# Optimization experiments

Hardware: AMD Instinct MI355X
Metric: run time of the kernel (lower is better)

Reference implementation:

```python
import jax, jax.numpy as jnp
import numpy as np

T, C, NH, NL, NP = 5, 192, 4, 5, 4
DH = C // NH

def leaky(x):
    return jnp.where(x >= 0, x, 0.1 * x)

def conv2d(x, w, b, padding=1, dilation=1):
    out = jax.lax.conv_general_dilated(
        x, w, window_strides=(1, 1),
        padding=[(padding, padding), (padding, padding)],
        rhs_dilation=(dilation, dilation),
        dimension_numbers=('NCHW', 'OIHW', 'NCHW'))
    return out + b[None, :, None, None]

def grid_sample_border(img, gx, gy):
    # align_corners=True, padding_mode='border'; gx/gy normalized [-1,1], shape (B,H,W)
    B, Cc, H, W = img.shape
    x = jnp.clip((gx + 1.0) * 0.5 * (W - 1), 0.0, W - 1)
    y = jnp.clip((gy + 1.0) * 0.5 * (H - 1), 0.0, H - 1)
    x0 = jnp.floor(x); y0 = jnp.floor(y)
    wx = (x - x0).reshape(B, 1, -1); wy = (y - y0).reshape(B, 1, -1)
    flat = img.reshape(B, Cc, H * W)
    def g(yi, xi):
        xi = jnp.clip(xi, 0, W - 1).astype(jnp.int32)
        yi = jnp.clip(yi, 0, H - 1).astype(jnp.int32)
        return jnp.take_along_axis(flat, (yi * W + xi).reshape(B, 1, -1), axis=2)
    out = (g(y0, x0) * (1 - wx) * (1 - wy) + g(y0, x0 + 1) * wx * (1 - wy)
         + g(y0 + 1, x0) * (1 - wx) * wy + g(y0 + 1, x0 + 1) * wx * wy)
    return out.reshape(B, Cc, H, W)

def warp(x, flo):
    B, _, H, W = x.shape
    xx = jnp.arange(W, dtype=jnp.float32)[None, :] * jnp.ones((H, 1), jnp.float32)
    yy = jnp.arange(H, dtype=jnp.float32)[:, None] * jnp.ones((1, W), jnp.float32)
    gx = 2.0 * (xx[None] + flo[:, 0]) / max(W - 1, 1) - 1.0
    gy = 2.0 * (yy[None] + flo[:, 1]) / max(H - 1, 1) - 1.0
    return grid_sample_border(x, gx, gy)

def deform_sample(v_img, loc):
    # v_img (N,D,H,W); loc (N,Q,P,2) in [0,1]; bilinear, zeros padding, align_corners=False
    N, D, H, W = v_img.shape
    Q, P = loc.shape[1], loc.shape[2]
    x = loc[..., 0] * W - 0.5
    y = loc[..., 1] * H - 0.5
    x0 = jnp.floor(x); y0 = jnp.floor(y)
    wx = (x - x0).reshape(N, 1, -1); wy = (y - y0).reshape(N, 1, -1)
    flat = v_img.reshape(N, D, H * W)
    def g(yi, xi):
        valid = ((xi >= 0) & (xi <= W - 1) & (yi >= 0) & (yi <= H - 1)).astype(v_img.dtype)
        xi_c = jnp.clip(xi, 0, W - 1).astype(jnp.int32)
        yi_c = jnp.clip(yi, 0, H - 1).astype(jnp.int32)
        return jnp.take_along_axis(flat, (yi_c * W + xi_c).reshape(N, 1, -1), axis=2) * valid.reshape(N, 1, -1)
    out = (g(y0, x0) * (1 - wx) * (1 - wy) + g(y0, x0 + 1) * wx * (1 - wy)
         + g(y0 + 1, x0) * (1 - wx) * wy + g(y0 + 1, x0 + 1) * wx * wy)
    return out.reshape(N, D, Q, P)

def _forward(frame, srcframe, flow_forward, flow_backward,
             w_qk, b_qk, w_v, b_v, w_vproj, b_vproj, w_off, b_off,
             w_attn, b_attn, w_out, b_out, w_ff, b_ff,
             w_ffn1, b_ffn1, w_ffn2, b_ffn2):
    b, t, c, h, w = frame.shape
    ff01, ff12 = flow_forward[:, 0], flow_forward[:, 1]
    fb32, fb43 = flow_backward[:, 2], flow_backward[:, 3]
    ff02 = ff01 + warp(ff12, ff01)
    fb42 = fb43 + warp(fb32, fb43)
    warp02 = warp(frame[:, 0], ff02)
    warp12 = warp(frame[:, 1], ff12)
    warp32 = warp(frame[:, 3], fb32)
    warp42 = warp(frame[:, 4], fb42)
    qk_in = jnp.concatenate([warp02, warp12, frame[:, 2], warp32, warp42,
                             flow_forward.reshape(b, -1, h, w),
                             flow_backward.reshape(b, -1, h, w)], axis=1)
    queries = leaky(conv2d(qk_in, w_qk, b_qk)).reshape(b, t, c, h, w)
    value = leaky(conv2d(frame.reshape(b, t * c, h, w), w_v, b_v)).reshape(b, t, c, h, w)

    Lq = t * h * w
    q_tok = queries.transpose(0, 1, 3, 4, 2).reshape(b, Lq, c)
    v_tok = value.transpose(0, 1, 3, 4, 2).reshape(b, Lq, c)
    v_proj = (v_tok @ w_vproj.T + b_vproj).reshape(b, t, h * w, NH, DH)

    offs = (q_tok @ w_off.T + b_off).reshape(b, Lq, NH, NL, NP, 2)
    aw = (q_tok @ w_attn.T + b_attn).reshape(b, Lq, NH, NL * NP)
    aw = jax.nn.softmax(aw, axis=-1).reshape(b, Lq, NH, NL, NP)

    # reference points (all valid ratios are ones): ((x+0.5)/W, (y+0.5)/H)
    rx = (jnp.arange(w, dtype=frame.dtype) + 0.5) / w
    ry = (jnp.arange(h, dtype=frame.dtype) + 0.5) / h
    ref = jnp.stack(jnp.meshgrid(rx, ry, indexing='xy'), axis=-1).reshape(h * w, 2)
    ref = jnp.tile(ref, (t, 1))  # (Lq, 2)

    norm = jnp.array([w, h], dtype=frame.dtype)
    # flow-guided per-level displacement toward the center frame (level 2)
    zero = jnp.zeros_like(ff12)
    flows = jnp.stack([ff02, ff12, zero, fb32, fb42], axis=1)  # (b,NL,2,h,w)
    flow_norm = (flows / norm[None, None, :, None, None]).transpose(0, 1, 3, 4, 2).reshape(b, NL, h * w, 2)
    flow_norm = jnp.tile(flow_norm.transpose(0, 2, 1, 3), (1, t, 1, 1))  # (b,Lq,NL,2)

    loc = (ref[None, :, None, None, None, :]
           + offs / norm[None, None, None, None, None, :]
           + flow_norm[:, :, None, :, None, :])  # (b,Lq,NH,NL,NP,2)

    acc = jnp.zeros((b * NH, DH, Lq), dtype=frame.dtype)
    for l in range(NL):
        v_l = v_proj[:, l].transpose(0, 2, 3, 1).reshape(b * NH, DH, h, w)
        loc_l = loc[:, :, :, l].transpose(0, 2, 1, 3, 4).reshape(b * NH, Lq, NP, 2)
        samp = deform_sample(v_l, loc_l)  # (b*NH, DH, Lq, NP)
        w_l = aw[:, :, :, l].transpose(0, 2, 1, 3).reshape(b * NH, 1, Lq, NP)
        acc = acc + (samp * w_l).sum(-1)
    attn = acc.reshape(b, NH, DH, Lq).transpose(0, 3, 1, 2).reshape(b, Lq, c)
    attn = attn @ w_out.T + b_out

    out = attn.reshape(b, t, h, w, c).transpose(0, 1, 4, 2, 3).reshape(b * t, c, h, w)
    out = conv2d(out, w_ff, b_ff)
    out = out.reshape(b, t, c, h, w) + frame
    seq_in = jnp.concatenate([out.reshape(b * t, c, h, w), srcframe.reshape(b * t, c, h, w)], axis=1)
    ffn = conv2d(seq_in, w_ffn1, b_ffn1, padding=2, dilation=2)
    ffn = conv2d(leaky(ffn), w_ffn2, b_ffn2)
    out = out.reshape(b * t, c, h, w) + ffn
    return out.reshape(b, t, c, h, w)

def setup_inputs():
    key = jax.random.key(0)
    ks = jax.random.split(key, 16)
    B, H, W = 2, 64, 64
    s = 0.02
    d = {}
    d['frame'] = jax.random.normal(ks[0], (B, T, C, H, W), jnp.float32)
    d['srcframe'] = jax.random.normal(ks[1], (B, T, C, H, W), jnp.float32)
    d['flow_forward'] = jax.random.normal(ks[2], (B, 4, 2, H, W), jnp.float32)
    d['flow_backward'] = jax.random.normal(ks[3], (B, 4, 2, H, W), jnp.float32)
    cin_qk = T * C + 4 * (T - 1)
    d['w_qk'] = jax.random.normal(ks[4], (T * C, cin_qk, 3, 3), jnp.float32) * s
    d['b_qk'] = jnp.zeros((T * C,), jnp.float32)
    d['w_v'] = jax.random.normal(ks[5], (T * C, T * C, 3, 3), jnp.float32) * s
    d['b_v'] = jnp.zeros((T * C,), jnp.float32)
    d['w_vproj'] = jax.random.normal(ks[6], (C, C), jnp.float32) * s
    d['b_vproj'] = jnp.zeros((C,), jnp.float32)
    d['w_off'] = jax.random.normal(ks[7], (NH * NL * NP * 2, C), jnp.float32) * s
    d['b_off'] = jax.random.normal(ks[8], (NH * NL * NP * 2,), jnp.float32)
    d['w_attn'] = jax.random.normal(ks[9], (NH * NL * NP, C), jnp.float32) * s
    d['b_attn'] = jnp.zeros((NH * NL * NP,), jnp.float32)
    d['w_out'] = jax.random.normal(ks[10], (C, C), jnp.float32) * s
    d['b_out'] = jnp.zeros((C,), jnp.float32)
    d['w_ff'] = jax.random.normal(ks[11], (C, C, 3, 3), jnp.float32) * s
    d['b_ff'] = jnp.zeros((C,), jnp.float32)
    d['w_ffn1'] = jax.random.normal(ks[12], (C, 2 * C, 3, 3), jnp.float32) * s
    d['b_ffn1'] = jnp.zeros((C,), jnp.float32)
    d['w_ffn2'] = jax.random.normal(ks[13], (C, C, 3, 3), jnp.float32) * s
    d['b_ffn2'] = jnp.zeros((C,), jnp.float32)
    return d

def reference(frame, srcframe, flow_forward, flow_backward, w_qk, b_qk, w_v, b_v, w_vproj, b_vproj, w_off, b_off, w_attn, b_attn, w_out, b_out, w_ff, b_ff, w_ffn1, b_ffn1, w_ffn2, b_ffn2):
    out = _forward(frame, srcframe, flow_forward, flow_backward, w_qk, b_qk, w_v, b_v, w_vproj, b_vproj, w_off, b_off, w_attn, b_attn, w_out, b_out, w_ff, b_ff, w_ffn1, b_ffn1, w_ffn2, b_ffn2)
    return (out, srcframe)
```

## Files before the change

### kernel.cpp

```cpp
#include <hip/hip_runtime.h>


#define HWPX 4096
#define PPXN 4624
#define LQ   20480

typedef __attribute__((ext_vector_type(8))) short  short8;
typedef __attribute__((ext_vector_type(4))) short  short4v;
typedef __attribute__((ext_vector_type(4))) float  f32x4;

__device__ __forceinline__ unsigned short f2bf(float f) {
    unsigned u = __float_as_uint(f);
    unsigned r = (u + 0x7FFF + ((u >> 16) & 1)) >> 16;
    return (unsigned short)r;
}
__device__ __forceinline__ float bf2f(unsigned short s) {
    return __uint_as_float(((unsigned)s) << 16);
}

__device__ __forceinline__ void gl_lds16(const unsigned short* g, unsigned short* l) {
    __builtin_amdgcn_global_load_lds(
        (const __attribute__((address_space(1))) unsigned int*)g,
        (__attribute__((address_space(3))) unsigned int*)l, 16, 0, 0);
}

__device__ __forceinline__ float bsample(const float* __restrict__ p, float sx, float sy) {
    sx = fminf(fmaxf(sx, 0.f), 63.f);
    sy = fminf(fmaxf(sy, 0.f), 63.f);
    float x0 = floorf(sx), y0 = floorf(sy);
    int ix0 = (int)x0, iy0 = (int)y0;
    int ix1 = ix0 < 63 ? ix0 + 1 : 63;
    int iy1 = iy0 < 63 ? iy0 + 1 : 63;
    float wx = sx - x0, wy = sy - y0;
    float v00 = p[iy0*64+ix0], v01 = p[iy0*64+ix1];
    float v10 = p[iy1*64+ix0], v11 = p[iy1*64+ix1];
    return (v00*(1.f-wx) + v01*wx)*(1.f-wy) + (v10*(1.f-wx) + v11*wx)*wy;
}

__global__ __launch_bounds__(256) void k_flow(const float* __restrict__ ff,
                                              const float* __restrict__ fb,
                                              float* __restrict__ flows) {
    int i = blockIdx.x*256 + threadIdx.x;
    int b = i >> 12, pix = i & 4095;
    int x = pix & 63, y = pix >> 6;
    const float* ff01 = ff + (size_t)(b*4+0)*2*HWPX;
    const float* ff12 = ff + (size_t)(b*4+1)*2*HWPX;
    const float* fb32 = fb + (size_t)(b*4+2)*2*HWPX;
    const float* fb43 = fb + (size_t)(b*4+3)*2*HWPX;
    float* F = flows + (size_t)b*5*2*HWPX;
    float ax = ff01[pix], ay = ff01[HWPX+pix];
    float sx = bsample(ff12,      (float)x+ax, (float)y+ay);
    float sy = bsample(ff12+HWPX, (float)x+ax, (float)y+ay);
    F[0*2*HWPX + pix]        = ax + sx;
    F[0*2*HWPX + HWPX + pix] = ay + sy;
    F[1*2*HWPX + pix]        = ff12[pix];
    F[1*2*HWPX + HWPX + pix] = ff12[HWPX+pix];
    F[2*2*HWPX + pix]        = 0.f;
    F[2*2*HWPX + HWPX + pix] = 0.f;
    F[3*2*HWPX + pix]        = fb32[pix];
    F[3*2*HWPX + HWPX + pix] = fb32[HWPX+pix];
    float bx = fb43[pix], by = fb43[HWPX+pix];
    float tx = bsample(fb32,      (float)x+bx, (float)y+by);
    float ty = bsample(fb32+HWPX, (float)x+bx, (float)y+by);
    F[4*2*HWPX + pix]        = bx + tx;
    F[4*2*HWPX + HWPX + pix] = by + ty;
}

__global__ void k_qkin(const unsigned short* __restrict__ Pv,
                       const float* __restrict__ ff, const float* __restrict__ fb,
                       const float* __restrict__ flows,
                       unsigned short* __restrict__ Pqk)
{
    int ppx = blockIdx.x*64 + threadIdx.x;
    if (ppx >= PPXN) return;
    int b = blockIdx.z;
    int c8 = (blockIdx.y*4 + threadIdx.y)*8;
    unsigned short* dst = Pqk + ((size_t)b*PPXN + ppx)*992 + c8;
    int py = ppx/68, pxc = ppx - py*68;
    short8 o = {};
    if (py >= 2 && py < 66 && pxc >= 2 && pxc < 66 && c8 < 976) {
        int y = py-2, x = pxc-2, pix = (y<<6)+x;
        if (c8 >= 960) {
            #pragma unroll
            for (int j = 0; j < 8; ++j) {
                int k = c8 - 960 + j;
                float v = (k < 8) ? ff[((size_t)b*8 + k)*HWPX + pix]
                                  : fb[((size_t)b*8 + k - 8)*HWPX + pix];
                o[j] = (short)f2bf(v);
            }
        } else {
            const unsigned short* Pvb = Pv + (size_t)b*PPXN*960;
            int slot = c8/192;
            if (slot == 2) {
                o = *(const short8*)(Pvb + (size_t)ppx*960 + c8);
            } else {
                const float* F = flows + ((size_t)(b*5 + slot)*2)*HWPX;
                float sx = fminf(fmaxf((float)x + F[pix], 0.f), 63.f);
                float sy = fminf(fmaxf((float)y + F[HWPX + pix], 0.f), 63.f);
                float x0 = floorf(sx), y0 = floorf(sy);
                int ix0 = (int)x0, iy0 = (int)y0;
                int ix1 = ix0 < 63 ? ix0+1 : 63, iy1 = iy0 < 63 ? iy0+1 : 63;
                float wx = sx - x0, wy = sy - y0;
                float w00 = (1.f-wx)*(1.f-wy), w01 = wx*(1.f-wy);
                float w10 = (1.f-wx)*wy,       w11 = wx*wy;
                short8 v00 = *(const short8*)(Pvb + ((size_t)((iy0+2)*68 + ix0+2))*960 + c8);
                short8 v01 = *(const short8*)(Pvb + ((size_t)((iy0+2)*68 + ix1+2))*960 + c8);
                short8 v10 = *(const short8*)(Pvb + ((size_t)((iy1+2)*68 + ix0+2))*960 + c8);
                short8 v11 = *(const short8*)(Pvb + ((size_t)((iy1+2)*68 + ix1+2))*960 + c8);
                #pragma unroll
                for (int j = 0; j < 8; ++j) {
                    float v = bf2f((unsigned short)v00[j])*w00 + bf2f((unsigned short)v01[j])*w01
                            + bf2f((unsigned short)v10[j])*w10 + bf2f((unsigned short)v11[j])*w11;
                    o[j] = (short)f2bf(v);
                }
            }
        }
    }
    *(short8*)dst = o;
}

__global__ void t_pad(const float* __restrict__ in, unsigned short* __restrict__ outb,
                      int CI, int PITCH, int COFF)
{
    int ppx = blockIdx.x*64 + threadIdx.x;
    if (ppx >= PPXN) return;
    int img = blockIdx.z;
    int c8 = (blockIdx.y*4 + threadIdx.y)*8;
    unsigned short* dst = outb + ((size_t)img*PPXN + ppx)*PITCH;
    int py = ppx/68, pxc = ppx - py*68;
    if (py < 2 || py >= 66 || pxc < 2 || pxc >= 66) {
        short8 z = {};
        *(short8*)(dst + c8) = z;
        if (COFF) *(short8*)(dst + COFF + c8) = z;
        return;
    }
    int pix = ((py-2)<<6) + (pxc-2);
    short8 o;
    #pragma unroll
    for (int j = 0; j < 8; ++j)
        o[j] = (short)f2bf(in[((size_t)img*CI + c8 + j)*HWPX + pix]);
    *(short8*)(dst + COFF + c8) = o;
}

__global__ __launch_bounds__(256) void t_zb(unsigned short* __restrict__ buf, int PITCH) {
    int id = blockIdx.x*256 + threadIdx.x;
    int perpx = PITCH >> 3;
    int ppx = id / perpx, c8 = (id - ppx*perpx) * 8;
    if (ppx >= PPXN) return;
    int py = ppx/68, pxc = ppx - py*68;
    if (py >= 2 && py < 66 && pxc >= 2 && pxc < 66) return;
    short8 z = {};
    *(short8*)(buf + ((size_t)blockIdx.y*PPXN + ppx)*PITCH + c8) = z;
}

__global__ __launch_bounds__(256) void t_wT(const float* __restrict__ w,
                                            unsigned short* __restrict__ wT,
                                            int CI, int NKB) {
    int cotile = blockIdx.x, kblk = blockIdx.y;
    int tid = threadIdx.x & 255;
    unsigned short* dst = wT + ((size_t)(cotile*NKB + kblk))*18432;
    #pragma unroll
    for (int it = 0; it < 9; ++it) {
        int idx = it*256 + tid;
        int tap = idx >> 8, sub = idx & 255;
        int cg = sub >> 6, co = sub & 63;
        int cog = cotile*64 + co;
        int ci0 = kblk*32 + cg*8;
        short8 v;
        #pragma unroll
        for (int j = 0; j < 8; ++j) {
            int ci = ci0 + j;
            v[j] = (ci < CI) ? (short)f2bf(w[((size_t)cog*CI + ci)*9 + tap]) : (short)0;
        }
        *(short8*)(dst + (size_t)idx*8) = v;
    }
}

__global__ __launch_bounds__(256) void t_wg(const float* __restrict__ w1,
                                            const float* __restrict__ w2,
                                            unsigned short* __restrict__ wg,
                                            int co_split, int CO) {
    int cotile = blockIdx.x;
    int tid = threadIdx.x & 255;
    unsigned short* dst = wg + (size_t)cotile*12288;
    #pragma unroll
    for (int it = 0; it < 6; ++it) {
        int idx = it*256 + tid;
        int kblk = idx >> 8, sub = idx & 255;
        int cg = sub >> 6, co = sub & 63;
        int cog = cotile*64 + co;
        int ci0 = kblk*32 + cg*8;
        short8 v = {};
        if (cog < CO) {
            const float* row = (cog < co_split) ? w1 + (size_t)cog*192
                                                : w2 + (size_t)(cog - co_split)*192;
            #pragma unroll
            for (int j = 0; j < 8; ++j) v[j] = (short)f2bf(row[ci0 + j]);
        }
        *(short8*)(dst + (size_t)idx*8) = v;
    }
}

template<int ROWS, int DIL, int OMODE>
__global__ __launch_bounds__(256) void k_conv(
    const unsigned short* __restrict__ P0, const unsigned short* __restrict__ P1,
    int CIP0, int CIP1, int NKB0, int NKB1,
    const unsigned short* __restrict__ wT0, const unsigned short* __restrict__ wT1,
    const float* __restrict__ bias0, const float* __restrict__ bias1,
    const float* __restrict__ res, float* __restrict__ outF,
    unsigned short* __restrict__ outB0, unsigned short* __restrict__ outB1,
    int njobs, int CO)
{
    constexpr int RR    = ROWS*4 + 2*DIL;
    constexpr int XP    = 64 + 2*DIL;
    constexpr int PLANE = RR*XP*16;
    constexpr int NCH   = RR*XP*4;
    constexpr int NXS   = (NCH + 255)/256;
    __shared__ unsigned char  s_x[2][4*PLANE];
    __shared__ unsigned short s_w[2][18432];

    int tid = threadIdx.x & 255;
    int cotile = blockIdx.x, ytile = blockIdx.y;
    int z = blockIdx.z;
    int sel = (njobs == 2) ? (z >> 1) : 0;
    int img = (njobs == 2) ? (z & 1)  : z;
    const unsigned short* P  = sel ? P1  : P0;
    const unsigned short* wT = sel ? wT1 : wT0;
    const float* bias        = sel ? bias1 : bias0;
    unsigned short* outB     = sel ? outB1 : outB0;
    int CIP = sel ? CIP1 : CIP0;
    int NKB = sel ? NKB1 : NKB0;

    int y0 = ytile * (ROWS*4);
    const unsigned short* Pi = P + (size_t)img*PPXN*CIP;
    int w = tid >> 6, lane = tid & 63, lm = lane & 15, cig = lane >> 4;

    auto stage_x = [&](int kb, int buf) {
        int k0 = kb*32;
        #pragma unroll
        for (int it = 0; it < NXS; ++it) {
            int li = it*256 + tid;
            if (li < NCH) {
                int p = li / (RR*XP), rem = li - p*(RR*XP);
                int r = rem / XP, c = rem - r*XP;
                gl_lds16(Pi + ((size_t)((y0 + 2 - DIL + r)*68 + c + 2 - DIL))*CIP + k0 + p*8,
                         (unsigned short*)&s_x[buf][li*16]);
            }
        }
    };
    auto stage_w = [&](int kb, int buf) {
        const unsigned short* ws = wT + ((size_t)(cotile*NKB + kb))*18432;
        #pragma unroll
        for (int it = 0; it < 9; ++it)
            gl_lds16(ws + (size_t)(it*256+tid)*8, &s_w[buf][(it*256+tid)*8]);
    };

    stage_x(0, 0); stage_w(0, 0);
    __syncthreads();

    f32x4 acc[4][ROWS*4] = {};
    int buf = 0;
    for (int kb = 0; kb < NKB; ++kb) {
        if (kb + 1 < NKB) { stage_x(kb+1, buf^1); stage_w(kb+1, buf^1); }
        #pragma unroll
        for (int t = 0; t < 9; ++t) {
            int ky = t/3, kx = t - ky*3;
            short8 A[4];
            #pragma unroll
            for (int mb = 0; mb < 4; ++mb)
                A[mb] = *(const short8*)&s_w[buf][((t*4 + cig)*64 + mb*16 + lm)*8];
            #pragma unroll
            for (int s = 0; s < ROWS; ++s) {
                short8 Bf[4];
                #pragma unroll
                for (int nc = 0; nc < 4; ++nc)
                    Bf[nc] = *(const short8*)&s_x[buf][cig*PLANE +
                               ((w*ROWS + s + ky*DIL)*XP + nc*16 + lm + kx*DIL)*16];
                #pragma unroll
                for (int mb = 0; mb < 4; ++mb)
                    #pragma unroll
                    for (int nc = 0; nc < 4; ++nc)
                        acc[mb][s*4+nc] = __builtin_amdgcn_mfma_f32_16x16x32_bf16(
                            A[mb], Bf[nc], acc[mb][s*4+nc], 0, 0, 0);
            }
        }
        __syncthreads();
        buf ^= 1;
    }

    #pragma unroll
    for (int mb = 0; mb < 4; ++mb) {
        int cob = cotile*64 + mb*16 + cig*4;
        #pragma unroll
        for (int s = 0; s < ROWS; ++s) {
            int y = y0 + w*ROWS + s;
            #pragma unroll
            for (int nc = 0; nc < 4; ++nc) {
                int x = nc*16 + lm;
                int px = (y<<6) + x;
                float vv[4];
                #pragma unroll
                for (int r = 0; r < 4; ++r) {
                    float v = acc[mb][s*4+nc][r] + bias[cob + r];
                    if (OMODE == 0 || OMODE == 2) v = v >= 0.f ? v : 0.1f*v;
                    if (OMODE == 1 || OMODE == 3)
                        v += res[((size_t)img*192 + cob + r)*HWPX + px];
                    vv[r] = v;
                }
                if (OMODE == 0) {
                    int it = cob/192, cc = cob - it*192;
                    short4v sv;
                    #pragma unroll
                    for (int r = 0; r < 4; ++r) sv[r] = (short)f2bf(vv[r]);
                    *(short4v*)(outB + (((size_t)(img*5 + it)*HWPX + px)*192 + cc)) = sv;
                } else if (OMODE == 1) {
                    #pragma unroll
                    for (int r = 0; r < 4; ++r)
                        outF[((size_t)img*192 + cob + r)*HWPX + px] = vv[r];
                    int ppx = ((px>>6)+2)*68 + (px&63) + 2;
                    short4v sv;
                    #pragma unroll
                    for (int r = 0; r < 4; ++r) sv[r] = (short)f2bf(vv[r]);
                    *(short4v*)(outB + ((size_t)img*PPXN + ppx)*384 + cob) = sv;
                } else if (OMODE == 2) {
                    int ppx = ((px>>6)+2)*68 + (px&63) + 2;
                    short4v sv;
                    #pragma unroll
                    for (int r = 0; r < 4; ++r) sv[r] = (short)f2bf(vv[r]);
                    *(short4v*)(outB + ((size_t)img*PPXN + ppx)*192 + cob) = sv;
                } else {
                    #pragma unroll
                    for (int r = 0; r < 4; ++r)
                        outF[((size_t)img*192 + cob + r)*HWPX + px] = vv[r];
                }
            }
        }
    }
}

template<int GMODE>
__global__ __launch_bounds__(256) void k_gemmm(
    const unsigned short* __restrict__ X, const unsigned short* __restrict__ WG,
    const float* __restrict__ b1, const float* __restrict__ b2,
    float* __restrict__ o1, float* __restrict__ o2, unsigned short* __restrict__ ob)
{
    __shared__ unsigned char  s_x[2][4*4096];
    __shared__ unsigned short s_w[12288];
    int tid = threadIdx.x & 255;
    int cotile = blockIdx.x, pxt = blockIdx.y, img = blockIdx.z;
    int px0 = pxt*256;
    const unsigned short* Xi = X + (size_t)img*HWPX*192;
    #pragma unroll
    for (int it = 0; it < 6; ++it)
        gl_lds16(WG + (size_t)cotile*12288 + (it*256+tid)*8, &s_w[(it*256+tid)*8]);
    short8 xr[4];
    #pragma unroll
    for (int it = 0; it < 4; ++it)
        xr[it] = *(const short8*)(Xi + (size_t)(px0 + tid)*192 + it*8);
    #pragma unroll
    for (int it = 0; it < 4; ++it)
        *(short8*)&s_x[0][it*4096 + tid*16] = xr[it];
    __syncthreads();
    int w = tid >> 6, lane = tid & 63, lm = lane & 15, cig = lane >> 4;
    f32x4 acc[4][4] = {};
    int xb = 0;
    for (int kb = 0; kb < 6; ++kb) {
        bool pf = (kb < 5);
        if (pf) {
            int k0 = (kb+1)*32;
            #pragma unroll
            for (int it = 0; it < 4; ++it)
                xr[it] = *(const short8*)(Xi + (size_t)(px0 + tid)*192 + k0 + it*8);
        }
        short8 A[4], Bf[4];
        #pragma unroll
        for (int nb = 0; nb < 4; ++nb)
            Bf[nb] = *(const short8*)&s_x[xb][cig*4096 + (w*64 + nb*16 + lm)*16];
        #pragma unroll
        for (int mb = 0; mb < 4; ++mb)
            A[mb] = *(const short8*)&s_w[((kb*4 + cig)*64 + mb*16 + lm)*8];
        #pragma unroll
        for (int mb = 0; mb < 4; ++mb)
            #pragma unroll
            for (int nb = 0; nb < 4; ++nb)
                acc[mb][nb] = __builtin_amdgcn_mfma_f32_16x16x32_bf16(
                    A[mb], Bf[nb], acc[mb][nb], 0, 0, 0);
        if (pf) {
            #pragma unroll
            for (int it = 0; it < 4; ++it)
                *(short8*)&s_x[xb^1][it*4096 + tid*16] = xr[it];
        }
        __syncthreads();
        xb ^= 1;
    }
    int b = img/5, t = img - b*5;
    #pragma unroll
    for (int mb = 0; mb < 4; ++mb) {
        int cob = cotile*64 + mb*16 + cig*4;
        if (GMODE == 1 && cob >= 240) continue;
        #pragma unroll
        for (int nb = 0; nb < 4; ++nb) {
            int px = px0 + w*64 + nb*16 + lm;
            float vv[4];
            #pragma unroll
            for (int r = 0; r < 4; ++r) {
                float bv;
                if (GMODE == 1) bv = (cob + r < 160) ? b1[cob+r] : b2[cob+r-160];
                else bv = b1[cob + r];
                vv[r] = acc[mb][nb][r] + bv;
            }
            if (GMODE == 0) {
                int h = cob/48, d = cob - h*48;
                short4v s;
                #pragma unroll
                for (int r = 0; r < 4; ++r) s[r] = (short)f2bf(vv[r]);
                *(short4v*)(ob + (((size_t)img*4 + h)*HWPX + px)*48 + d) = s;
            } else if (GMODE == 1) {
                #pragma unroll
                for (int r = 0; r < 4; ++r) {
                    int co = cob + r;
                    if (co < 160) o1[((size_t)b*160 + co)*LQ + t*HWPX + px] = vv[r];
                    else          o2[((size_t)b*80 + co-160)*LQ + t*HWPX + px] = vv[r];
                }
            } else {
                int ppx = ((px>>6)+2)*68 + (px&63) + 2;
                short4v s;
                #pragma unroll
                for (int r = 0; r < 4; ++r) s[r] = (short)f2bf(vv[r]);
                *(short4v*)(ob + ((size_t)img*PPXN + ppx)*192 + cob) = s;
            }
        }
    }
}

__global__ __launch_bounds__(256) void k_softmax20(float* __restrict__ aw) {
    int i = blockIdx.x*256 + threadIdx.x;
    int lq = i % LQ;
    int bh = i / LQ;
    float* p = aw + (size_t)bh*20*LQ + lq;
    float e[20];
    float m = -1e30f;
    #pragma unroll
    for (int j = 0; j < 20; ++j) { e[j] = p[(size_t)j*LQ]; m = fmaxf(m, e[j]); }
    float s = 0.f;
    #pragma unroll
    for (int j = 0; j < 20; ++j) { e[j] = expf(e[j]-m); s += e[j]; }
    float inv = 1.f/s;
    #pragma unroll
    for (int j = 0; j < 20; ++j) p[(size_t)j*LQ] = e[j]*inv;
}

__device__ __forceinline__ void addtap(float* acc, const unsigned short* __restrict__ src, float w) {
    const short8* s8 = (const short8*)src;
    #pragma unroll
    for (int q = 0; q < 6; ++q) {
        short8 v = s8[q];
        #pragma unroll
        for (int j = 0; j < 8; ++j)
            acc[q*8+j] += w * bf2f((unsigned short)v[j]);
    }
}

__global__ __launch_bounds__(256) void k_sample(
    const unsigned short* __restrict__ vp, const float* __restrict__ offs,
    const float* __restrict__ aw, const float* __restrict__ flows,
    unsigned short* __restrict__ accout)
{
    int blk = blockIdx.x;
    int b = blk / 320, sub = blk - b*320;
    int h = threadIdx.x >> 6;
    int lq = sub*64 + (threadIdx.x & 63);
    int pix = lq & 4095;
    int x = pix & 63, y = pix >> 6;
    const float* offp = offs + ((size_t)b*160 + h*40)*LQ + lq;
    const float* awp  = aw   + ((size_t)b*80  + h*20)*LQ + lq;
    float acc[48];
    #pragma unroll
    for (int d = 0; d < 48; ++d) acc[d] = 0.f;

    for (int l = 0; l < 5; ++l) {
        float fx = flows[((size_t)(b*5+l)*2+0)*HWPX + pix];
        float fy = flows[((size_t)(b*5+l)*2+1)*HWPX + pix];
        const unsigned short* vpl = vp + ((size_t)(b*5+l)*4 + h)*HWPX*48;
        #pragma unroll
        for (int p = 0; p < 4; ++p) {
            int o = l*4 + p;
            float ox = offp[(size_t)(2*o)*LQ];
            float oy = offp[(size_t)(2*o+1)*LQ];
            float wv = awp[(size_t)o*LQ];
            float sx = (float)x + ox + fx;
            float sy = (float)y + oy + fy;
            float x0f = floorf(sx), y0f = floorf(sy);
            float wx = sx - x0f, wy = sy - y0f;
            int ix0 = (int)x0f, iy0 = (int)y0f;
            float w00 = wv*(1.f-wx)*(1.f-wy), w01 = wv*wx*(1.f-wy);
            float w10 = wv*(1.f-wx)*wy,       w11 = wv*wx*wy;
            bool vx0 = (ix0 >= 0)  && (ix0 <= 63);
            bool vx1 = (ix0 >= -1) && (ix0 <= 62);
            bool vy0 = (iy0 >= 0)  && (iy0 <= 63);
            bool vy1 = (iy0 >= -1) && (iy0 <= 62);
            if (vy0 && vx0) addtap(acc, vpl + (size_t)(iy0*64 + ix0)*48,       w00);
            if (vy0 && vx1) addtap(acc, vpl + (size_t)(iy0*64 + ix0 + 1)*48,   w01);
            if (vy1 && vx0) addtap(acc, vpl + (size_t)((iy0+1)*64 + ix0)*48,   w10);
            if (vy1 && vx1) addtap(acc, vpl + (size_t)((iy0+1)*64 + ix0+1)*48, w11);
        }
    }
    unsigned short* dst = accout + ((size_t)b*LQ + lq)*192 + h*48;
    #pragma unroll
    for (int q = 0; q < 6; ++q) {
        short8 s;
        #pragma unroll
        for (int j = 0; j < 8; ++j) s[j] = (short)f2bf(acc[q*8+j]);
        *(short8*)(dst + q*8) = s;
    }
}


extern "C" void kernel_launch(void* const* d_in, const int* in_sizes, int n_in,
                              void* d_out, int out_size, void* d_ws, size_t ws_size,
                              hipStream_t stream) {
    (void)in_sizes; (void)n_in; (void)out_size; (void)ws_size;
    const float* frame    = (const float*)d_in[0];
    const float* srcframe = (const float*)d_in[1];
    const float* flow_f   = (const float*)d_in[2];
    const float* flow_b   = (const float*)d_in[3];
    const float* w_qk  = (const float*)d_in[4];  const float* b_qk  = (const float*)d_in[5];
    const float* w_v   = (const float*)d_in[6];  const float* b_v   = (const float*)d_in[7];
    const float* w_vp  = (const float*)d_in[8];  const float* b_vp  = (const float*)d_in[9];
    const float* w_off = (const float*)d_in[10]; const float* b_off = (const float*)d_in[11];
    const float* w_at  = (const float*)d_in[12]; const float* b_at  = (const float*)d_in[13];
    const float* w_out = (const float*)d_in[14]; const float* b_out = (const float*)d_in[15];
    const float* w_ff  = (const float*)d_in[16]; const float* b_ff  = (const float*)d_in[17];
    const float* w_f1  = (const float*)d_in[18]; const float* b_f1  = (const float*)d_in[19];
    const float* w_f2  = (const float*)d_in[20]; const float* b_f2  = (const float*)d_in[21];
    float* out = (float*)d_out;
    char* W = (char*)d_ws;

    float*          flows  = (float*)(W + 0);
    unsigned short* wT_qk  = (unsigned short*)(W + 327680);
    unsigned short* wT_v   = (unsigned short*)(W + 17469440);
    unsigned short* wT_ff  = (unsigned short*)(W + 327680);
    unsigned short* wT_f1  = (unsigned short*)(W + 991232);
    unsigned short* wT_f2  = (unsigned short*)(W + 2318336);
    unsigned short* wg_vp  = (unsigned short*)(W + 2981888);
    unsigned short* wg_oa  = (unsigned short*)(W + 3055616);
    unsigned short* wg_out = (unsigned short*)(W + 3153920);
    unsigned short* P_qk   = (unsigned short*)(W + 34058240);
    unsigned short* P_ff   = P_qk;
    unsigned short* P_v    = (unsigned short*)(W + 52406272);
    unsigned short* P_mid  = P_v;
    unsigned short* Q_tok  = (unsigned short*)(W + 70162432);
    unsigned short* acc_tok= Q_tok;
    unsigned short* V_tok  = (unsigned short*)(W + 85891072);
    unsigned short* P_ffn1 = V_tok;
    unsigned short* vp     = (unsigned short*)(W + 101619712);
    float*          offs   = (float*)(W + 121403392);
    float*          aw     = (float*)(W + 147617792);
    float*          out1   = (float*)(W + 160724992);

    dim3 bp(64, 4);

    k_flow<<<32, 256, 0, stream>>>(flow_f, flow_b, flows);
    t_wT<<<dim3(15,31), 256, 0, stream>>>(w_qk, wT_qk, 976, 31);
    t_wT<<<dim3(15,30), 256, 0, stream>>>(w_v,  wT_v,  960, 30);
    t_pad<<<dim3(73,30,2), bp, 0, stream>>>(frame, P_v, 960, 960, 0);
    k_qkin<<<dim3(73,31,2), bp, 0, stream>>>(P_v, flow_f, flow_b, flows, P_qk);
    k_conv<2,1,0><<<dim3(15,8,4), 256, 0, stream>>>(
        P_qk, P_v, 992, 960, 31, 30, wT_qk, wT_v, b_qk, b_v,
        nullptr, nullptr, Q_tok, V_tok, 2, 960);
    t_wT<<<dim3(3,6),  256, 0, stream>>>(w_ff, wT_ff, 192, 6);
    t_wT<<<dim3(3,12), 256, 0, stream>>>(w_f1, wT_f1, 384, 12);
    t_wT<<<dim3(3,6),  256, 0, stream>>>(w_f2, wT_f2, 192, 6);
    t_wg<<<3, 256, 0, stream>>>(w_vp,  nullptr, wg_vp, 192, 192);
    t_wg<<<4, 256, 0, stream>>>(w_off, w_at,    wg_oa, 160, 240);
    t_wg<<<3, 256, 0, stream>>>(w_out, nullptr, wg_out, 192, 192);
    t_zb<<<dim3(434,10), 256, 0, stream>>>(P_ff, 192);
    t_zb<<<dim3(434,10), 256, 0, stream>>>(P_mid, 192);
    k_gemmm<0><<<dim3(3,16,10), 256, 0, stream>>>(V_tok, wg_vp, b_vp, nullptr,
                                                  nullptr, nullptr, vp);
    k_gemmm<1><<<dim3(4,16,10), 256, 0, stream>>>(Q_tok, wg_oa, b_off, b_at,
                                                  offs, aw, nullptr);
    k_softmax20<<<640, 256, 0, stream>>>(aw);
    k_sample<<<640, 256, 0, stream>>>(vp, offs, aw, flows, acc_tok);
    t_pad<<<dim3(73,6,10), bp, 0, stream>>>(srcframe, P_ffn1, 192, 384, 192);
    k_gemmm<2><<<dim3(3,16,10), 256, 0, stream>>>(acc_tok, wg_out, b_out, nullptr,
                                                  nullptr, nullptr, P_ff);
    k_conv<1,1,1><<<dim3(3,16,10), 256, 0, stream>>>(
        P_ff, nullptr, 192, 0, 6, 0, wT_ff, nullptr, b_ff, nullptr,
        frame, out1, P_ffn1, nullptr, 1, 192);
    k_conv<1,2,2><<<dim3(3,16,10), 256, 0, stream>>>(
        P_ffn1, nullptr, 384, 0, 12, 0, wT_f1, nullptr, b_f1, nullptr,
        nullptr, nullptr, P_mid, nullptr, 1, 192);
    k_conv<1,1,3><<<dim3(3,16,10), 256, 0, stream>>>(
        P_mid, nullptr, 192, 0, 6, 0, wT_f2, nullptr, b_f2, nullptr,
        out1, out, nullptr, nullptr, 1, 192);
    hipMemcpyAsync(out + (size_t)2*5*192*HWPX, srcframe,
                   (size_t)2*5*192*HWPX*sizeof(float),
                   hipMemcpyDeviceToDevice, stream);
}
```

Before: 964.1 us.

## Single-buffer conv LDS with register prefetch, 2-block occupancy, and XCD-aware block remap

The conv kernel's double-buffered LDS is replaced by a single buffer. The next input tile is now prefetched into registers during compute and written to LDS after a barrier, while the weights are staged with direct global-to-LDS loads after compute. This halves LDS use so that launch_bounds(256,2) can fit two blocks per CU. Block indices are also remapped so that consecutive blocks land on the same XCD, for better L2 locality. The cost is an extra barrier per k-step, weight loads that no longer overlap compute, and higher register pressure from the prefetch registers.

```diff
diff --git a/kernel.cpp b/kernel.cpp
--- a/kernel.cpp
+++ b/kernel.cpp
@@ -202,7 +202,7 @@
 }
 
 template<int ROWS, int DIL, int OMODE>
-__global__ __launch_bounds__(256) void k_conv(
+__global__ __launch_bounds__(256, 2) void k_conv(
     const unsigned short* __restrict__ P0, const unsigned short* __restrict__ P1,
     int CIP0, int CIP1, int NKB0, int NKB1,
     const unsigned short* __restrict__ wT0, const unsigned short* __restrict__ wT1,
@@ -216,12 +216,17 @@
     constexpr int PLANE = RR*XP*16;
     constexpr int NCH   = RR*XP*4;
     constexpr int NXS   = (NCH + 255)/256;
-    __shared__ unsigned char  s_x[2][4*PLANE];
-    __shared__ unsigned short s_w[2][18432];
+    __shared__ unsigned char  s_x[4*PLANE];
+    __shared__ unsigned short s_w[18432];
 
     int tid = threadIdx.x & 255;
-    int cotile = blockIdx.x, ytile = blockIdx.y;
-    int z = blockIdx.z;
+    int gx = gridDim.x, gy = gridDim.y, gz = gridDim.z;
+    int lin = blockIdx.x + gx*(blockIdx.y + gy*blockIdx.z);
+    int tot = gx*gy*gz;
+    if ((tot & 7) == 0) { int q = tot >> 3; lin = (lin & 7)*q + (lin >> 3); }
+    int cotile = lin % gx; int rem = lin / gx;
+    int ytile = rem % gy;  int z = rem / gy;
+
     int sel = (njobs == 2) ? (z >> 1) : 0;
     int img = (njobs == 2) ? (z & 1)  : z;
     const unsigned short* P  = sel ? P1  : P0;
@@ -235,46 +240,57 @@
     const unsigned short* Pi = P + (size_t)img*PPXN*CIP;
     int w = tid >> 6, lane = tid & 63, lm = lane & 15, cig = lane >> 4;
 
-    auto stage_x = [&](int kb, int buf) {
+    short8 xr[NXS];
+    auto load_x = [&](int kb) {
         int k0 = kb*32;
         #pragma unroll
         for (int it = 0; it < NXS; ++it) {
             int li = it*256 + tid;
             if (li < NCH) {
-                int p = li / (RR*XP), rem = li - p*(RR*XP);
-                int r = rem / XP, c = rem - r*XP;
-                gl_lds16(Pi + ((size_t)((y0 + 2 - DIL + r)*68 + c + 2 - DIL))*CIP + k0 + p*8,
-                         (unsigned short*)&s_x[buf][li*16]);
+                int p = li / (RR*XP), rm = li - p*(RR*XP);
+                int r = rm / XP, c = rm - r*XP;
+                xr[it] = *(const short8*)(Pi +
+                    ((size_t)((y0 + 2 - DIL + r)*68 + c + 2 - DIL))*CIP + k0 + p*8);
             }
         }
     };
-    auto stage_w = [&](int kb, int buf) {
+    auto write_x = [&]() {
+        #pragma unroll
+        for (int it = 0; it < NXS; ++it) {
+            int li = it*256 + tid;
+            if (li < NCH) {
+                int p = li / (RR*XP), rm = li - p*(RR*XP);
+                *(short8*)&s_x[p*PLANE + rm*16] = xr[it];
+            }
+        }
+    };
+    auto stage_w = [&](int kb) {
         const unsigned short* ws = wT + ((size_t)(cotile*NKB + kb))*18432;
         #pragma unroll
         for (int it = 0; it < 9; ++it)
-            gl_lds16(ws + (size_t)(it*256+tid)*8, &s_w[buf][(it*256+tid)*8]);
+            gl_lds16(ws + (size_t)(it*256+tid)*8, &s_w[(it*256+tid)*8]);
     };
 
-    stage_x(0, 0); stage_w(0, 0);
+    load_x(0); stage_w(0); write_x();
     __syncthreads();
 
     f32x4 acc[4][ROWS*4] = {};
-    int buf = 0;
     for (int kb = 0; kb < NKB; ++kb) {
-        if (kb + 1 < NKB) { stage_x(kb+1, buf^1); stage_w(kb+1, buf^1); }
+        bool pf = (kb + 1 < NKB);
+        if (pf) load_x(kb+1);
         #pragma unroll
         for (int t = 0; t < 9; ++t) {
             int ky = t/3, kx = t - ky*3;
             short8 A[4];
             #pragma unroll
             for (int mb = 0; mb < 4; ++mb)
-                A[mb] = *(const short8*)&s_w[buf][((t*4 + cig)*64 + mb*16 + lm)*8];
+                A[mb] = *(const short8*)&s_w[((t*4 + cig)*64 + mb*16 + lm)*8];
             #pragma unroll
             for (int s = 0; s < ROWS; ++s) {
                 short8 Bf[4];
                 #pragma unroll
                 for (int nc = 0; nc < 4; ++nc)
-                    Bf[nc] = *(const short8*)&s_x[buf][cig*PLANE +
+                    Bf[nc] = *(const short8*)&s_x[cig*PLANE +
                                ((w*ROWS + s + ky*DIL)*XP + nc*16 + lm + kx*DIL)*16];
                 #pragma unroll
                 for (int mb = 0; mb < 4; ++mb)
@@ -285,7 +301,8 @@
             }
         }
         __syncthreads();
-        buf ^= 1;
+        if (pf) { stage_w(kb+1); write_x(); }
+        __syncthreads();
     }
 
     #pragma unroll
```

New measurement: 871.3 us. -9.6%, faster.
